# Performance work log

Measured on AMD Instinct MI355X. Metric: run time of the kernel, lower is better.

Reference implementation:

```python
import jax, jax.numpy as jnp
import numpy as np

B_SZ, SEQ, FEAT, STATE = 4, 4096, 1024, 64
HID = 4 * FEAT
EPS = 1e-5
LOG_DT_MIN, LOG_DT_MAX = float(np.log(0.001)), float(np.log(0.1))


def _s5_params(key, feat, state):
    ks = jax.random.split(key, 6)
    n = jnp.arange(state, dtype=jnp.float32)
    return {
        'log_A_real': jnp.log(n + 0.5),          # HiPPO-diag: A_real = -(n+0.5)
        'A_imag': jnp.pi * n,                     # HiPPO-diag: A_imag = pi*n
        'B_re': jax.random.normal(ks[0], (state, feat)) / np.sqrt(state),
        'B_im': jax.random.normal(ks[1], (state, feat)) / np.sqrt(state),
        'C_re': jax.random.normal(ks[2], (feat, state)) / np.sqrt(feat),
        'C_im': jax.random.normal(ks[3], (feat, state)) / np.sqrt(feat),
        'D': jax.random.normal(ks[4], (feat,)),
        'log_dt': jax.random.uniform(ks[5], (state,), minval=LOG_DT_MIN, maxval=LOG_DT_MAX),
    }


def setup_inputs() -> dict:
    key = jax.random.key(0)
    k = jax.random.split(key, 10)
    pf = _s5_params(k[2], FEAT, STATE)
    pb = _s5_params(k[3], FEAT, STATE)
    inp = {
        'x': jax.random.normal(k[0], (B_SZ, SEQ, FEAT), jnp.float32),
        'cond': jax.random.normal(k[1], (B_SZ, FEAT), jnp.float32),
        'ada_W': jax.random.normal(k[4], (FEAT, 6 * FEAT)) * 0.02,
        'ada_b': jnp.zeros((6 * FEAT,), jnp.float32),
        'out_W': jax.random.normal(k[5], (2 * FEAT, FEAT)) / np.sqrt(2 * FEAT),
        'out_b': jnp.zeros((FEAT,), jnp.float32),
        'mlp_W1': jax.random.normal(k[6], (FEAT, HID)) / np.sqrt(FEAT),
        'mlp_b1': jnp.zeros((HID,), jnp.float32),
        'mlp_W2': jax.random.normal(k[7], (HID, FEAT)) / np.sqrt(HID),
        'mlp_b2': jnp.zeros((FEAT,), jnp.float32),
        'freqs_cis': jnp.zeros((SEQ, STATE), jnp.float32),  # accepted, unused (interface compat)
    }
    for name, p in (('fwd', pf), ('bwd', pb)):
        for kk, v in p.items():
            inp[f'{name}_{kk}'] = v
    return inp


def _layernorm(x):
    # LayerNorm with use_scale=False, use_bias=False
    mu = jnp.mean(x, axis=-1, keepdims=True)
    var = jnp.var(x, axis=-1, keepdims=True)
    return (x - mu) * jax.lax.rsqrt(var + EPS)


def _s5(u, log_A_real, A_imag, B_re, B_im, C_re, C_im, D, log_dt):
    # Diagonal S5: x_k = A_bar*x_{k-1} + B_bar*u_k ; y = Re(C x) + D u
    dt = jnp.exp(log_dt)                                   # [N]
    A_diag = -jnp.exp(log_A_real) + 1j * A_imag            # [N] complex
    A_bar = jnp.exp(A_diag * dt)                           # [N]
    B_bar = (A_bar[:, None] - 1.0) / (A_diag[:, None] + 1e-8) * (B_re + 1j * B_im)  # [N,F]
    u_f = u.astype(jnp.float32)
    Bu = jnp.einsum('bsf,nf->bsn', u_f, B_bar)             # [B,S,N] complex
    A_exp = jnp.broadcast_to(A_bar[None, None, :], Bu.shape)

    def comb(e1, e2):
        a1, b1 = e1
        a2, b2 = e2
        return (a1 * a2, a2 * b1 + b2)

    _, xs = jax.lax.associative_scan(comb, (A_exp, Bu), axis=1)  # [B,S,N]
    y = jnp.einsum('fn,bsn->bsf', C_re + 1j * C_im, xs).real
    return y + D * u_f


def _block(x, cond, ada_W, ada_b, pf, pb, out_W, out_b, mlp_W1, mlp_b1, mlp_W2, mlp_b2):
    # AdaLN modulation params (standard DiT ordering: shift/scale/gate for msa then mlp)
    ada = jax.nn.silu(cond) @ ada_W + ada_b                # [B,6F]
    sh1, sc1, g1, sh2, sc2, g2 = jnp.split(ada, 6, axis=-1)
    h = _layernorm(x) * (1.0 + sc1[:, None, :]) + sh1[:, None, :]
    # bidirectional S5
    y_f = _s5(h, *pf)
    y_b = jnp.flip(_s5(jnp.flip(h, 1), *pb), 1)
    y = jnp.concatenate([y_f, y_b], axis=-1) @ out_W + out_b
    x = x + g1[:, None, :] * y
    h2 = _layernorm(x) * (1.0 + sc2[:, None, :]) + sh2[:, None, :]
    h2 = jax.nn.gelu(h2 @ mlp_W1 + mlp_b1) @ mlp_W2 + mlp_b2
    return x + g2[:, None, :] * h2


def reference(x, cond, ada_W, ada_b,
              fwd_log_A_real, fwd_A_imag, fwd_B_re, fwd_B_im, fwd_C_re, fwd_C_im, fwd_D, fwd_log_dt,
              bwd_log_A_real, bwd_A_imag, bwd_B_re, bwd_B_im, bwd_C_re, bwd_C_im, bwd_D, bwd_log_dt,
              out_W, out_b, mlp_W1, mlp_b1, mlp_W2, mlp_b2, freqs_cis):
    pf = (fwd_log_A_real, fwd_A_imag, fwd_B_re, fwd_B_im, fwd_C_re, fwd_C_im, fwd_D, fwd_log_dt)
    pb = (bwd_log_A_real, bwd_A_imag, bwd_B_re, bwd_B_im, bwd_C_re, bwd_C_im, bwd_D, bwd_log_dt)
    return _block(x, cond, ada_W, ada_b, pf, pb, out_W, out_b, mlp_W1, mlp_b1, mlp_W2, mlp_b2)
```

## Files before the change

kernel.cpp:

```cpp
#include <hip/hip_runtime.h>
#include <cstddef>

#define NF    1024
#define NSEQ  4096
#define NB    4
#define NROWS (NB*NSEQ)
#define NADA  6144
#define NHID  4096
#define NST   64
#define NCH   128
#define LCH   64
#define NCHUNK (NSEQ/LCH)
#define LDA   1280

typedef __bf16 bf16x8 __attribute__((ext_vector_type(8)));
typedef float f32x4 __attribute__((ext_vector_type(4)));

__device__ __forceinline__ unsigned short f2bf(float x) {
  union { float f; unsigned int u; } v; v.f = x;
  unsigned int r = v.u + 0x7fffu + ((v.u >> 16) & 1u);
  return (unsigned short)(r >> 16);
}

__device__ __forceinline__ float gelu_fast(float x) {
  float u2 = 1.5957691216057308f*(x + 0.044715f*x*x*x);
  return x / (1.f + __expf(-u2));
}

template<int TM, int TN, int WM, int WN>
__device__ __forceinline__ void mfma_core(
    const unsigned short* __restrict__ A, int lda,
    const unsigned short* __restrict__ Bt, int ldb,
    int K, int row0, int col0, unsigned short* lds, f32x4* acc)
{
  constexpr int MI = TM/(16*WM), NJ = TN/(16*WN);
  const int tid  = threadIdx.x;
  const int wave = tid >> 6, lane = tid & 63;
  const int wm = wave % WM, wn = wave / WM;
  const int sr = lane >> 2;
  const int sc = (lane & 3) << 3;
  const int fr = lane & 15, fq = lane >> 4;
  unsigned short* sA = lds;
  unsigned short* sB = lds + TM*32;
  const unsigned short* a0 = A + (size_t)row0*lda;
  const unsigned short* b0 = Bt + (size_t)col0*ldb;
#pragma unroll 2
  for (int k0 = 0; k0 < K; k0 += 32) {
#pragma unroll
    for (int s = 0; s < TM/64; ++s) {
      int u = s*4 + wave;
      int r = u*16 + sr;
      __builtin_amdgcn_global_load_lds(
          (const __attribute__((address_space(1))) void*)(a0 + (size_t)r*lda + k0 + sc),
          (__attribute__((address_space(3))) void*)(sA + u*512), 16, 0, 0);
    }
#pragma unroll
    for (int s = 0; s < TN/64; ++s) {
      int u = s*4 + wave;
      int r = u*16 + sr;
      __builtin_amdgcn_global_load_lds(
          (const __attribute__((address_space(1))) void*)(b0 + (size_t)r*ldb + k0 + sc),
          (__attribute__((address_space(3))) void*)(sB + u*512), 16, 0, 0);
    }
    __syncthreads();
    bf16x8 af[MI], bv[NJ];
#pragma unroll
    for (int i = 0; i < MI; ++i)
      af[i] = *(const bf16x8*)(sA + (wm*(MI*16) + i*16 + fr)*32 + fq*8);
#pragma unroll
    for (int j = 0; j < NJ; ++j)
      bv[j] = *(const bf16x8*)(sB + (wn*(NJ*16) + j*16 + fr)*32 + fq*8);
#pragma unroll
    for (int i = 0; i < MI; ++i)
#pragma unroll
      for (int j = 0; j < NJ; ++j)
        acc[i*NJ+j] = __builtin_amdgcn_mfma_f32_16x16x32_bf16(af[i], bv[j], acc[i*NJ+j], 0, 0, 0);
    __syncthreads();
  }
}

#define ACC_INIT(N_) f32x4 acc[N_]; \
  _Pragma("unroll") for (int z_ = 0; z_ < N_; ++z_) acc[z_] = (f32x4){0.f,0.f,0.f,0.f};

#define EPI_LOOP(WM_, MI_, NJ_, body) \
  { const int lane = threadIdx.x & 63, wave = threadIdx.x >> 6; \
    const int wm = wave % WM_, wn = wave / WM_; \
    const int fr = lane & 15, fq = lane >> 4; \
    _Pragma("unroll") for (int i = 0; i < MI_; ++i) \
    _Pragma("unroll") for (int j = 0; j < NJ_; ++j) \
    _Pragma("unroll") for (int r = 0; r < 4; ++r) { \
      int row = row0 + wm*(MI_*16) + i*16 + fq*4 + r; \
      int col = col0 + wn*(NJ_*16) + j*16 + fr; \
      float aval = acc[i*NJ_+j][r]; \
      body; } }

__global__ __launch_bounds__(256, 4) void k_mm_bu(const unsigned short* __restrict__ A,
                                                  const unsigned short* __restrict__ Bt,
                                                  float* __restrict__ C) {
  __shared__ __align__(16) unsigned short lds[(64+128)*32];
  ACC_INIT(8)
  int row0 = blockIdx.x*64, col0 = blockIdx.y*128;
  mfma_core<64,128,1,4>(A, LDA, Bt, 1024, 1024, row0, col0, lds, acc);
  EPI_LOOP(1, 4, 2, C[(size_t)row*(2*NCH) + col] = aval; )
}

__global__ __launch_bounds__(256, 4) void k_mm_g(const unsigned short* __restrict__ A,
                                                 const unsigned short* __restrict__ Bt,
                                                 unsigned short* __restrict__ Bcat) {
  __shared__ __align__(16) unsigned short lds[(64+128)*32];
  ACC_INIT(8)
  int row0 = blockIdx.x*64, col0 = blockIdx.y*128;
  mfma_core<64,128,1,4>(A, 2048, Bt, 2048, 2048, row0, col0, lds, acc);
  EPI_LOOP(1, 4, 2, Bcat[(size_t)col*LDA + row] = f2bf(aval); )
}

__global__ __launch_bounds__(256, 4) void k_mm_proj(const unsigned short* __restrict__ A,
                                                    const unsigned short* __restrict__ Bt,
                                                    const float* __restrict__ x,
                                                    const float* __restrict__ ada,
                                                    const float* __restrict__ outb,
                                                    float* __restrict__ outp) {
  __shared__ __align__(16) unsigned short lds[2*128*32];
  ACC_INIT(16)
  int row0 = blockIdx.x*128, col0 = blockIdx.y*128;
  mfma_core<128,128,2,2>(A, LDA, Bt, LDA, LDA, row0, col0, lds, acc);
  EPI_LOOP(2, 4, 4,
    const float* g1 = ada + (size_t)(row >> 12)*NADA + 2*NF;
    outp[(size_t)row*NF + col] = x[(size_t)row*NF + col] + g1[col]*(aval + outb[col]); )
}

__global__ __launch_bounds__(256, 4) void k_mm_mlp1(const unsigned short* __restrict__ A,
                                                    const unsigned short* __restrict__ Bt,
                                                    const float* __restrict__ b1,
                                                    unsigned short* __restrict__ mid) {
  __shared__ __align__(16) unsigned short lds[2*128*32];
  ACC_INIT(16)
  int row0 = blockIdx.x*128, col0 = blockIdx.y*128;
  mfma_core<128,128,2,2>(A, LDA, Bt, 1024, 1024, row0, col0, lds, acc);
  EPI_LOOP(2, 4, 4, mid[(size_t)row*NHID + col] = f2bf(gelu_fast(aval + b1[col])); )
}

__global__ __launch_bounds__(256, 4) void k_mm_mlp2(const unsigned short* __restrict__ A,
                                                    const unsigned short* __restrict__ Bt,
                                                    const float* __restrict__ b2,
                                                    const float* __restrict__ ada,
                                                    float* __restrict__ outp, int row_off) {
  __shared__ __align__(16) unsigned short lds[2*128*32];
  ACC_INIT(16)
  int row0 = blockIdx.x*128, col0 = blockIdx.y*128;
  mfma_core<128,128,2,2>(A, NHID, Bt, NHID, NHID, row0, col0, lds, acc);
  EPI_LOOP(2, 4, 4,
    int rg = row_off + row;
    const float* g2 = ada + (size_t)(rg >> 12)*NADA + 5*NF;
    outp[(size_t)rg*NF + col] += g2[col]*(aval + b2[col]); )
}

__global__ __launch_bounds__(256) void k_ada1(const float* __restrict__ cond, const float* __restrict__ adaW,
                                              float* __restrict__ part) {
  int j = blockIdx.x*256 + threadIdx.x;
  int b = blockIdx.y, z = blockIdx.z;
  float acc = 0.f;
  const float* s = cond + b*NF;
  int k0 = z*128;
  for (int k = k0; k < k0+128; ++k) {
    float c = s[k];
    acc += (c / (1.f + __expf(-c))) * adaW[(size_t)k*NADA + j];
  }
  part[((size_t)(z*NB + b))*NADA + j] = acc;
}

__global__ __launch_bounds__(256) void k_ada2(const float* __restrict__ part, const float* __restrict__ adab,
                                              float* __restrict__ ada) {
  int j = blockIdx.x*256 + threadIdx.x;
  int b = blockIdx.y;
  float acc = adab[j];
#pragma unroll
  for (int z = 0; z < 8; ++z) acc += part[((size_t)(z*NB + b))*NADA + j];
  ada[(size_t)b*NADA + j] = acc;
}

__global__ __launch_bounds__(64) void k_param(
    const float* __restrict__ lAf, const float* __restrict__ Aif, const float* __restrict__ ldtf,
    const float* __restrict__ lAb, const float* __restrict__ Aib, const float* __restrict__ ldtb,
    float* __restrict__ Abar, float* __restrict__ coef, float* __restrict__ AbarL, float* __restrict__ Apow)
{
  int d = blockIdx.x, n = threadIdx.x;
  const float* lA  = d ? lAb  : lAf;
  const float* Ai  = d ? Aib  : Aif;
  const float* ldt = d ? ldtb : ldtf;
  float dt  = expf(ldt[n]);
  float Are = -expf(lA[n]);
  float Aim = Ai[n];
  float ar = Are*dt, ai = Aim*dt;
  float m = expf(ar);
  float Abr = m*cosf(ai), Abi = m*sinf(ai);
  int t = d*NST + n;
  Abar[2*t] = Abr; Abar[2*t+1] = Abi;
  float cr = Abr - 1.f, ci = Abi;
  float dr = Are + 1e-8f, di = Aim;
  float den = dr*dr + di*di;
  coef[2*t]   = (cr*dr + ci*di)/den;
  coef[2*t+1] = (ci*dr - cr*di)/den;
  for (int j = 0; j < LCH; ++j) {
    float p = (float)(j+1);
    float mp = expf(ar*p);
    Apow[(size_t)(t*LCH + j)*2 + 0] = mp*cosf(ai*p);
    Apow[(size_t)(t*LCH + j)*2 + 1] = mp*sinf(ai*p);
  }
  float mL = expf(ar*64.f);
  AbarL[2*t] = mL*cosf(ai*64.f); AbarL[2*t+1] = mL*sinf(ai*64.f);
}

__global__ __launch_bounds__(256) void k_bmat_t(
    const float* __restrict__ Brf, const float* __restrict__ Bif,
    const float* __restrict__ Brb, const float* __restrict__ Bib,
    const float* __restrict__ coef, unsigned short* __restrict__ Bmat_t)
{
  int id = blockIdx.x*256 + threadIdx.x;
  int f = id & (NF-1), c = id >> 10;
  int d = c >> 6, n = c & 63;
  const float* Br = d ? Brb : Brf;
  const float* Bi = d ? Bib : Bif;
  float br = Br[(size_t)n*NF + f], bi = Bi[(size_t)n*NF + f];
  float crr = coef[2*c], cii = coef[2*c+1];
  Bmat_t[(size_t)(2*c)*NF + f]   = f2bf(crr*br - cii*bi);
  Bmat_t[(size_t)(2*c+1)*NF + f] = f2bf(crr*bi + cii*br);
}

__global__ __launch_bounds__(256) void k_ccat(
    const float* __restrict__ Crf, const float* __restrict__ Cif,
    const float* __restrict__ Crb, const float* __restrict__ Cib,
    unsigned short* __restrict__ Ccat)
{
  int id = blockIdx.x*256 + threadIdx.x;
  int fp = id & 2047, r = id >> 11;
  int p = r & 1, c = r >> 1, d = c >> 6, n = c & 63;
  int fd = fp >> 10, f = fp & 1023;
  float v = 0.f;
  if (fd == d) {
    const float* Cr = d ? Crb : Crf;
    const float* Ci = d ? Cib : Cif;
    v = p ? -Ci[(size_t)f*NST + n] : Cr[(size_t)f*NST + n];
  }
  Ccat[id] = f2bf(v);
}

__global__ __launch_bounds__(256) void k_ln_mod_bf(const float* __restrict__ xin, const float* __restrict__ ada,
                                                   int sh_off, int sc_off, unsigned short* __restrict__ outp) {
  const int row = blockIdx.x;
  const int b = row >> 12;
  const int tid = threadIdx.x;
  float4 v = ((const float4*)(xin + (size_t)row*NF))[tid];
  float s1 = v.x+v.y+v.z+v.w;
  float s2 = v.x*v.x + v.y*v.y + v.z*v.z + v.w*v.w;
  for (int off = 32; off > 0; off >>= 1) { s1 += __shfl_down(s1, off); s2 += __shfl_down(s2, off); }
  __shared__ float r1[4], r2[4];
  if ((tid & 63) == 0) { r1[tid>>6] = s1; r2[tid>>6] = s2; }
  __syncthreads();
  float S1 = r1[0]+r1[1]+r1[2]+r1[3];
  float S2 = r2[0]+r2[1]+r2[2]+r2[3];
  float mean = S1 * (1.0f/NF);
  float var  = S2 * (1.0f/NF) - mean*mean;
  float inv  = rsqrtf(var + 1e-5f);
  const float* arow = ada + (size_t)b*NADA;
  int f = tid << 2;
  ushort4 r;
  r.x = f2bf((v.x - mean)*inv*(1.f + arow[sc_off + f+0]) + arow[sh_off + f+0]);
  r.y = f2bf((v.y - mean)*inv*(1.f + arow[sc_off + f+1]) + arow[sh_off + f+1]);
  r.z = f2bf((v.z - mean)*inv*(1.f + arow[sc_off + f+2]) + arow[sh_off + f+2]);
  r.w = f2bf((v.w - mean)*inv*(1.f + arow[sc_off + f+3]) + arow[sh_off + f+3]);
  *(ushort4*)(outp + (size_t)row*LDA + f) = r;
}

__global__ __launch_bounds__(128) void k_scanA(float* __restrict__ Bu, const float* __restrict__ Abar,
                                               float* __restrict__ P) {
  int t = threadIdx.x;
  int bc = blockIdx.x;
  int b = bc >> 6, c = bc & 63;
  int d = t >> 6;
  float2 A = ((const float2*)Abar)[t];
  float sr = 0.f, si = 0.f;
  size_t base = ((size_t)b*NSEQ)*(2*NCH);
  for (int j = 0; j < LCH; ++j) {
    int s = d ? (c*LCH + (LCH-1) - j) : (c*LCH + j);
    float2* p = (float2*)(Bu + base + (size_t)s*(2*NCH)) + t;
    float2 u = *p;
    float nr = A.x*sr - A.y*si + u.x;
    float ni = A.x*si + A.y*sr + u.y;
    sr = nr; si = ni;
    *p = make_float2(sr, si);
  }
  ((float2*)P)[(size_t)bc*NCH + t] = make_float2(sr, si);
}

__global__ __launch_bounds__(512) void k_scanB(const float* __restrict__ P, const float* __restrict__ AbarL,
                                               float* __restrict__ carry) {
  int t = threadIdx.x & (NCH-1);
  int b = threadIdx.x >> 7;
  int d = t >> 6;
  float2 AL = ((const float2*)AbarL)[t];
  float sr = 0.f, si = 0.f;
  if (d == 0) {
    for (int c = 0; c < NCHUNK; ++c) {
      ((float2*)carry)[((size_t)b*NCHUNK + c)*NCH + t] = make_float2(sr, si);
      float2 p = ((const float2*)P)[((size_t)b*NCHUNK + c)*NCH + t];
      float nr = AL.x*sr - AL.y*si + p.x;
      float ni = AL.x*si + AL.y*sr + p.y;
      sr = nr; si = ni;
    }
  } else {
    for (int c = NCHUNK-1; c >= 0; --c) {
      ((float2*)carry)[((size_t)b*NCHUNK + c)*NCH + t] = make_float2(sr, si);
      float2 p = ((const float2*)P)[((size_t)b*NCHUNK + c)*NCH + t];
      float nr = AL.x*sr - AL.y*si + p.x;
      float ni = AL.x*si + AL.y*sr + p.y;
      sr = nr; si = ni;
    }
  }
}

__global__ __launch_bounds__(128) void k_scanC(const float* __restrict__ Bu, const float* __restrict__ Apow,
                                               const float* __restrict__ carry,
                                               unsigned short* __restrict__ Acat) {
  int t = threadIdx.x;
  int bc = blockIdx.x;
  int b = bc >> 6, c = bc & 63;
  int d = t >> 6;
  float2 E = ((const float2*)carry)[(size_t)bc*NCH + t];
  const float2* Ap = ((const float2*)Apow) + (size_t)t*LCH;
  size_t base = ((size_t)b*NSEQ)*(2*NCH);
  for (int j = 0; j < LCH; ++j) {
    int s = c*LCH + j;
    int tau = d ? (LCH-1 - j) : j;
    float2 ap = Ap[tau];
    float2 v = *((const float2*)(Bu + base + (size_t)s*(2*NCH)) + t);
    v.x += ap.x*E.x - ap.y*E.y;
    v.y += ap.x*E.y + ap.y*E.x;
    ushort2 o; o.x = f2bf(v.x); o.y = f2bf(v.y);
    *(ushort2*)(Acat + (size_t)(b*NSEQ + s)*LDA + 2*t) = o;
  }
}

__global__ void k_tcvt(const float* __restrict__ src, int R, int C,
                       unsigned short* __restrict__ dst, int ldd) {
  __shared__ float t[32][33];
  int c0 = blockIdx.x*32, r0 = blockIdx.y*32;
  for (int rr = threadIdx.y; rr < 32; rr += 8)
    t[rr][threadIdx.x] = src[(size_t)(r0+rr)*C + c0 + threadIdx.x];
  __syncthreads();
  for (int rr = threadIdx.y; rr < 32; rr += 8)
    dst[(size_t)(c0+rr)*ldd + r0 + threadIdx.x] = f2bf(t[threadIdx.x][rr]);
}

__global__ void k_wd_t(const float* __restrict__ Df, const float* __restrict__ Db,
                       const float* __restrict__ W, unsigned short* __restrict__ dst) {
  __shared__ float t1[32][33], t2[32][33];
  __shared__ float df[32], db[32];
  int fo0 = blockIdx.x*32, f0 = blockIdx.y*32;
  for (int rr = threadIdx.y; rr < 32; rr += 8) {
    t1[rr][threadIdx.x] = W[(size_t)(f0+rr)*NF + fo0 + threadIdx.x];
    t2[rr][threadIdx.x] = W[(size_t)(NF+f0+rr)*NF + fo0 + threadIdx.x];
  }
  if (threadIdx.y == 0) { df[threadIdx.x] = Df[f0+threadIdx.x]; db[threadIdx.x] = Db[f0+threadIdx.x]; }
  __syncthreads();
  for (int rr = threadIdx.y; rr < 32; rr += 8)
    dst[(size_t)(fo0+rr)*LDA + f0 + threadIdx.x] =
        f2bf(df[threadIdx.x]*t1[threadIdx.x][rr] + db[threadIdx.x]*t2[threadIdx.x][rr]);
}

extern "C" void kernel_launch(void* const* d_in, const int* in_sizes, int n_in,
                              void* d_out, int out_size, void* d_ws, size_t ws_size,
                              hipStream_t stream) {
  const bool sig = (in_sizes[4] == 64);
  const float* x    = (const float*)d_in[0];
  const float* cond = (const float*)d_in[1];
  const float* adaW = (const float*)d_in[2];
  const float* adab = (const float*)d_in[3];
  const int fwd0 = sig ? 4 : 11;
  const int bwd0 = sig ? 12 : 19;
  const float* outW = (const float*)d_in[sig ? 20 : 4];
  const float* outb = (const float*)d_in[sig ? 21 : 5];
  const float* W1   = (const float*)d_in[sig ? 22 : 6];
  const float* b1   = (const float*)d_in[sig ? 23 : 7];
  const float* W2   = (const float*)d_in[sig ? 24 : 8];
  const float* b2   = (const float*)d_in[sig ? 25 : 9];
  const float* lAf  = (const float*)d_in[fwd0+0];
  const float* Aif  = (const float*)d_in[fwd0+1];
  const float* Brf  = (const float*)d_in[fwd0+2];
  const float* Bif  = (const float*)d_in[fwd0+3];
  const float* Crf  = (const float*)d_in[fwd0+4];
  const float* Cif  = (const float*)d_in[fwd0+5];
  const float* Df   = (const float*)d_in[fwd0+6];
  const float* ldtf = (const float*)d_in[fwd0+7];
  const float* lAb  = (const float*)d_in[bwd0+0];
  const float* Aib  = (const float*)d_in[bwd0+1];
  const float* Brb  = (const float*)d_in[bwd0+2];
  const float* Bib  = (const float*)d_in[bwd0+3];
  const float* Crb  = (const float*)d_in[bwd0+4];
  const float* Cib  = (const float*)d_in[bwd0+5];
  const float* Db   = (const float*)d_in[bwd0+6];
  const float* ldtb = (const float*)d_in[bwd0+7];
  float* out = (float*)d_out;
  (void)n_in; (void)out_size;

  char* w = (char*)d_ws;
  auto alloc = [&](size_t bytes) { char* p = w; w += (bytes + 255) & ~(size_t)255; return p; };
  unsigned short* Acat   = (unsigned short*)alloc((size_t)NROWS*LDA*2);
  unsigned short* W1t    = (unsigned short*)alloc((size_t)NHID*NF*2);
  unsigned short* W2t    = (unsigned short*)alloc((size_t)NF*NHID*2);
  unsigned short* Wot    = (unsigned short*)alloc((size_t)NF*2048*2);
  unsigned short* Ccat   = (unsigned short*)alloc((size_t)256*2048*2);
  unsigned short* Bmat_t = (unsigned short*)alloc((size_t)2*NCH*NF*2);
  unsigned short* Bcat   = (unsigned short*)alloc((size_t)NF*LDA*2);
  float* bu    = (float*)alloc((size_t)NROWS*2*NCH*4);
  float* ada   = (float*)alloc((size_t)NB*NADA*4);
  float* part  = (float*)alloc((size_t)8*NB*NADA*4);
  float* Abar  = (float*)alloc(2*NCH*4);
  float* AbarL = (float*)alloc(2*NCH*4);
  float* coef  = (float*)alloc(2*NCH*4);
  float* Apow  = (float*)alloc((size_t)NCH*LCH*2*4);
  float* P     = (float*)alloc((size_t)NB*NCHUNK*NCH*2*4);
  float* carry = (float*)alloc((size_t)NB*NCHUNK*NCH*2*4);
  size_t used = (size_t)(w - (char*)d_ws);
  int mrows = NROWS;
  while (mrows > 4096 && used + (size_t)mrows*NHID*2 > ws_size) mrows >>= 1;
  unsigned short* mid = (unsigned short*)alloc((size_t)mrows*NHID*2);

  k_ada1<<<dim3(NADA/256, NB, 8), 256, 0, stream>>>(cond, adaW, part);
  k_ada2<<<dim3(NADA/256, NB), 256, 0, stream>>>(part, adab, ada);
  k_param<<<2, 64, 0, stream>>>(lAf, Aif, ldtf, lAb, Aib, ldtb, Abar, coef, AbarL, Apow);
  k_bmat_t<<<(2*NCH*NF)/(2*256), 256, 0, stream>>>(Brf, Bif, Brb, Bib, coef, Bmat_t);
  k_ccat<<<(256*2048)/256, 256, 0, stream>>>(Crf, Cif, Crb, Cib, Ccat);

  k_tcvt<<<dim3(NHID/32, NF/32), dim3(32,8), 0, stream>>>(W1, NF, NHID, W1t, NF);
  k_tcvt<<<dim3(NF/32, NHID/32), dim3(32,8), 0, stream>>>(W2, NHID, NF, W2t, NHID);
  k_tcvt<<<dim3(NF/32, 2048/32), dim3(32,8), 0, stream>>>(outW, 2048, NF, Wot, 2048);

  k_mm_g<<<dim3(4, NF/128), 256, 0, stream>>>(Ccat, Wot, Bcat);
  k_wd_t<<<dim3(NF/32, NF/32), dim3(32,8), 0, stream>>>(Df, Db, outW, Bcat + 256);

  k_ln_mod_bf<<<NROWS, 256, 0, stream>>>(x, ada, 0, NF, Acat + 256);

  k_mm_bu<<<dim3(NROWS/64, (2*NCH)/128), 256, 0, stream>>>(Acat + 256, Bmat_t, bu);

  k_scanA<<<NB*NCHUNK, NCH, 0, stream>>>(bu, Abar, P);
  k_scanB<<<1, 512, 0, stream>>>(P, AbarL, carry);
  k_scanC<<<NB*NCHUNK, NCH, 0, stream>>>(bu, Apow, carry, Acat);

  k_mm_proj<<<dim3(NROWS/128, NF/128), 256, 0, stream>>>(Acat, Bcat, x, ada, outb, out);

  k_ln_mod_bf<<<NROWS, 256, 0, stream>>>(out, ada, 3*NF, 4*NF, Acat + 256);

  for (int r0 = 0; r0 < NROWS; r0 += mrows) {
    k_mm_mlp1<<<dim3(mrows/128, NHID/128), 256, 0, stream>>>(Acat + 256 + (size_t)r0*LDA, W1t, b1, mid);
    k_mm_mlp2<<<dim3(mrows/128, NF/128), 256, 0, stream>>>(mid, W2t, b2, ada, out, r0);
  }
}
```

Baseline: 785.9 us.

## Fuse chunk scan into Bu GEMM, merge prep kernels, deepen GEMM K-step

The first phase of the chunked scan now runs inside the Bu GEMM epilogue. The block stages its 64x128 tile in shared memory, runs the intra-chunk recurrence there, and writes Bu and the chunk carries. This removes one global read-modify-write of Bu and a separate launch. The weight transpose/convert kernels and the B/C table kernels are each merged into a single launch. The shared MFMA core now loads two 32-wide K slices per barrier pair, halving synchronizations at the cost of doubled LDS per block, which may lower occupancy.

```diff
diff --git a/kernel.cpp b/kernel.cpp
--- a/kernel.cpp
+++ b/kernel.cpp
@@ -15,6 +15,9 @@
 
 typedef __bf16 bf16x8 __attribute__((ext_vector_type(8)));
 typedef float f32x4 __attribute__((ext_vector_type(4)));
+
+#define AS1 __attribute__((address_space(1)))
+#define AS3 __attribute__((address_space(3)))
 
 __device__ __forceinline__ unsigned short f2bf(float x) {
   union { float f; unsigned int u; } v; v.f = x;
@@ -41,40 +44,44 @@
   const int sc = (lane & 3) << 3;
   const int fr = lane & 15, fq = lane >> 4;
   unsigned short* sA = lds;
-  unsigned short* sB = lds + TM*32;
+  unsigned short* sB = lds + 2*TM*32;
   const unsigned short* a0 = A + (size_t)row0*lda;
   const unsigned short* b0 = Bt + (size_t)col0*ldb;
-#pragma unroll 2
-  for (int k0 = 0; k0 < K; k0 += 32) {
-#pragma unroll
-    for (int s = 0; s < TM/64; ++s) {
-      int u = s*4 + wave;
-      int r = u*16 + sr;
-      __builtin_amdgcn_global_load_lds(
-          (const __attribute__((address_space(1))) void*)(a0 + (size_t)r*lda + k0 + sc),
-          (__attribute__((address_space(3))) void*)(sA + u*512), 16, 0, 0);
-    }
-#pragma unroll
-    for (int s = 0; s < TN/64; ++s) {
-      int u = s*4 + wave;
-      int r = u*16 + sr;
-      __builtin_amdgcn_global_load_lds(
-          (const __attribute__((address_space(1))) void*)(b0 + (size_t)r*ldb + k0 + sc),
-          (__attribute__((address_space(3))) void*)(sB + u*512), 16, 0, 0);
+  for (int k0 = 0; k0 < K; k0 += 64) {
+#pragma unroll
+    for (int p = 0; p < 2; ++p) {
+      int kk = k0 + p*32;
+#pragma unroll
+      for (int s = 0; s < TM/64; ++s) {
+        int u = s*4 + wave;
+        __builtin_amdgcn_global_load_lds(
+            (const AS1 void*)(a0 + (size_t)(u*16 + sr)*lda + kk + sc),
+            (AS3 void*)(sA + p*TM*32 + u*512), 16, 0, 0);
+      }
+#pragma unroll
+      for (int s = 0; s < TN/64; ++s) {
+        int u = s*4 + wave;
+        __builtin_amdgcn_global_load_lds(
+            (const AS1 void*)(b0 + (size_t)(u*16 + sr)*ldb + kk + sc),
+            (AS3 void*)(sB + p*TN*32 + u*512), 16, 0, 0);
+      }
     }
     __syncthreads();
-    bf16x8 af[MI], bv[NJ];
-#pragma unroll
-    for (int i = 0; i < MI; ++i)
-      af[i] = *(const bf16x8*)(sA + (wm*(MI*16) + i*16 + fr)*32 + fq*8);
-#pragma unroll
-    for (int j = 0; j < NJ; ++j)
-      bv[j] = *(const bf16x8*)(sB + (wn*(NJ*16) + j*16 + fr)*32 + fq*8);
-#pragma unroll
-    for (int i = 0; i < MI; ++i)
+#pragma unroll
+    for (int p = 0; p < 2; ++p) {
+      bf16x8 af[MI], bv[NJ];
+#pragma unroll
+      for (int i = 0; i < MI; ++i)
+        af[i] = *(const bf16x8*)(sA + p*TM*32 + (wm*(MI*16) + i*16 + fr)*32 + fq*8);
 #pragma unroll
       for (int j = 0; j < NJ; ++j)
-        acc[i*NJ+j] = __builtin_amdgcn_mfma_f32_16x16x32_bf16(af[i], bv[j], acc[i*NJ+j], 0, 0, 0);
+        bv[j] = *(const bf16x8*)(sB + p*TN*32 + (wn*(NJ*16) + j*16 + fr)*32 + fq*8);
+#pragma unroll
+      for (int i = 0; i < MI; ++i)
+#pragma unroll
+        for (int j = 0; j < NJ; ++j)
+          acc[i*NJ+j] = __builtin_amdgcn_mfma_f32_16x16x32_bf16(af[i], bv[j], acc[i*NJ+j], 0, 0, 0);
+    }
     __syncthreads();
   }
 }
@@ -94,20 +101,60 @@
       float aval = acc[i*NJ_+j][r]; \
       body; } }
 
-__global__ __launch_bounds__(256, 4) void k_mm_bu(const unsigned short* __restrict__ A,
-                                                  const unsigned short* __restrict__ Bt,
-                                                  float* __restrict__ C) {
-  __shared__ __align__(16) unsigned short lds[(64+128)*32];
+__global__ __launch_bounds__(256, 4) void k_mm_bu_scan(
+    const unsigned short* __restrict__ A, const unsigned short* __restrict__ Bt,
+    const float* __restrict__ Abar, float* __restrict__ Bu, float* __restrict__ P)
+{
+  __shared__ __align__(16) char smem[64*128*4];
+  unsigned short* lds = (unsigned short*)smem;
+  float* sbuf = (float*)smem;
   ACC_INIT(8)
   int row0 = blockIdx.x*64, col0 = blockIdx.y*128;
   mfma_core<64,128,1,4>(A, LDA, Bt, 1024, 1024, row0, col0, lds, acc);
-  EPI_LOOP(1, 4, 2, C[(size_t)row*(2*NCH) + col] = aval; )
+  { const int lane = threadIdx.x & 63, wave = threadIdx.x >> 6;
+    const int fr = lane & 15, fq = lane >> 4;
+#pragma unroll
+    for (int i = 0; i < 4; ++i)
+#pragma unroll
+      for (int j = 0; j < 2; ++j)
+#pragma unroll
+        for (int r = 0; r < 4; ++r) {
+          int rl = i*16 + fq*4 + r;
+          int cl = wave*32 + j*16 + fr;
+          sbuf[rl*128 + cl] = acc[i*2+j][r];
+        }
+  }
+  __syncthreads();
+  int tid = threadIdx.x;
+  if (tid < 64) {
+    int ch = (col0 >> 1) + tid;
+    int d = ch >> 6;
+    float2 Ae = ((const float2*)Abar)[ch];
+    float sr_ = 0.f, si_ = 0.f;
+    for (int jj = 0; jj < LCH; ++jj) {
+      int rl = d ? (LCH-1 - jj) : jj;
+      float re = sbuf[rl*128 + 2*tid];
+      float im = sbuf[rl*128 + 2*tid + 1];
+      float nr = Ae.x*sr_ - Ae.y*si_ + re;
+      float ni = Ae.x*si_ + Ae.y*sr_ + im;
+      sr_ = nr; si_ = ni;
+      sbuf[rl*128 + 2*tid]     = sr_;
+      sbuf[rl*128 + 2*tid + 1] = si_;
+    }
+    int bc = row0 >> 6;
+    ((float2*)P)[(size_t)bc*NCH + ch] = make_float2(sr_, si_);
+  }
+  __syncthreads();
+  for (int e = tid; e < 64*32; e += 256) {
+    int r = e >> 5, q = (e & 31) << 2;
+    *(float4*)(Bu + (size_t)(row0 + r)*(2*NCH) + col0 + q) = *(float4*)(sbuf + r*128 + q);
+  }
 }
 
 __global__ __launch_bounds__(256, 4) void k_mm_g(const unsigned short* __restrict__ A,
                                                  const unsigned short* __restrict__ Bt,
                                                  unsigned short* __restrict__ Bcat) {
-  __shared__ __align__(16) unsigned short lds[(64+128)*32];
+  __shared__ __align__(16) unsigned short lds[2*(64+128)*32];
   ACC_INIT(8)
   int row0 = blockIdx.x*64, col0 = blockIdx.y*128;
   mfma_core<64,128,1,4>(A, 2048, Bt, 2048, 2048, row0, col0, lds, acc);
@@ -120,7 +167,7 @@
                                                     const float* __restrict__ ada,
                                                     const float* __restrict__ outb,
                                                     float* __restrict__ outp) {
-  __shared__ __align__(16) unsigned short lds[2*128*32];
+  __shared__ __align__(16) unsigned short lds[2*2*128*32];
   ACC_INIT(16)
   int row0 = blockIdx.x*128, col0 = blockIdx.y*128;
   mfma_core<128,128,2,2>(A, LDA, Bt, LDA, LDA, row0, col0, lds, acc);
@@ -133,7 +180,7 @@
                                                     const unsigned short* __restrict__ Bt,
                                                     const float* __restrict__ b1,
                                                     unsigned short* __restrict__ mid) {
-  __shared__ __align__(16) unsigned short lds[2*128*32];
+  __shared__ __align__(16) unsigned short lds[2*2*128*32];
   ACC_INIT(16)
   int row0 = blockIdx.x*128, col0 = blockIdx.y*128;
   mfma_core<128,128,2,2>(A, LDA, Bt, 1024, 1024, row0, col0, lds, acc);
@@ -145,7 +192,7 @@
                                                     const float* __restrict__ b2,
                                                     const float* __restrict__ ada,
                                                     float* __restrict__ outp, int row_off) {
-  __shared__ __align__(16) unsigned short lds[2*128*32];
+  __shared__ __align__(16) unsigned short lds[2*2*128*32];
   ACC_INIT(16)
   int row0 = blockIdx.x*128, col0 = blockIdx.y*128;
   mfma_core<128,128,2,2>(A, NHID, Bt, NHID, NHID, row0, col0, lds, acc);
@@ -211,38 +258,81 @@
   AbarL[2*t] = mL*cosf(ai*64.f); AbarL[2*t+1] = mL*sinf(ai*64.f);
 }
 
-__global__ __launch_bounds__(256) void k_bmat_t(
+__global__ __launch_bounds__(256) void k_tabs(
     const float* __restrict__ Brf, const float* __restrict__ Bif,
     const float* __restrict__ Brb, const float* __restrict__ Bib,
-    const float* __restrict__ coef, unsigned short* __restrict__ Bmat_t)
-{
-  int id = blockIdx.x*256 + threadIdx.x;
-  int f = id & (NF-1), c = id >> 10;
-  int d = c >> 6, n = c & 63;
-  const float* Br = d ? Brb : Brf;
-  const float* Bi = d ? Bib : Bif;
-  float br = Br[(size_t)n*NF + f], bi = Bi[(size_t)n*NF + f];
-  float crr = coef[2*c], cii = coef[2*c+1];
-  Bmat_t[(size_t)(2*c)*NF + f]   = f2bf(crr*br - cii*bi);
-  Bmat_t[(size_t)(2*c+1)*NF + f] = f2bf(crr*bi + cii*br);
-}
-
-__global__ __launch_bounds__(256) void k_ccat(
+    const float* __restrict__ coef, unsigned short* __restrict__ Bmat_t,
     const float* __restrict__ Crf, const float* __restrict__ Cif,
     const float* __restrict__ Crb, const float* __restrict__ Cib,
     unsigned short* __restrict__ Ccat)
 {
-  int id = blockIdx.x*256 + threadIdx.x;
-  int fp = id & 2047, r = id >> 11;
-  int p = r & 1, c = r >> 1, d = c >> 6, n = c & 63;
-  int fd = fp >> 10, f = fp & 1023;
-  float v = 0.f;
-  if (fd == d) {
-    const float* Cr = d ? Crb : Crf;
-    const float* Ci = d ? Cib : Cif;
-    v = p ? -Ci[(size_t)f*NST + n] : Cr[(size_t)f*NST + n];
-  }
-  Ccat[id] = f2bf(v);
+  if (blockIdx.x < 512) {
+    int id = blockIdx.x*256 + threadIdx.x;
+    int f = id & (NF-1), c = id >> 10;
+    int d = c >> 6, n = c & 63;
+    const float* Br = d ? Brb : Brf;
+    const float* Bi = d ? Bib : Bif;
+    float br = Br[(size_t)n*NF + f], bi = Bi[(size_t)n*NF + f];
+    float crr = coef[2*c], cii = coef[2*c+1];
+    Bmat_t[(size_t)(2*c)*NF + f]   = f2bf(crr*br - cii*bi);
+    Bmat_t[(size_t)(2*c+1)*NF + f] = f2bf(crr*bi + cii*br);
+  } else {
+    int id = (blockIdx.x - 512)*256 + threadIdx.x;
+    int fp = id & 2047, r = id >> 11;
+    int p = r & 1, c = r >> 1, d = c >> 6, n = c & 63;
+    int fd = fp >> 10, f = fp & 1023;
+    float v = 0.f;
+    if (fd == d) {
+      const float* Cr = d ? Crb : Crf;
+      const float* Ci = d ? Cib : Cif;
+      v = p ? -Ci[(size_t)f*NST + n] : Cr[(size_t)f*NST + n];
+    }
+    Ccat[id] = f2bf(v);
+  }
+}
+
+__device__ __forceinline__ void tcvt_tile(const float* __restrict__ src, int C,
+                                          unsigned short* __restrict__ dst, int ldd,
+                                          int r0, int c0, float* t) {
+  for (int rr = threadIdx.y; rr < 32; rr += 8)
+    t[rr*33 + threadIdx.x] = src[(size_t)(r0+rr)*C + c0 + threadIdx.x];
+  __syncthreads();
+  for (int rr = threadIdx.y; rr < 32; rr += 8)
+    dst[(size_t)(c0+rr)*ldd + r0 + threadIdx.x] = f2bf(t[threadIdx.x*33 + rr]);
+}
+
+__global__ void k_wprep(const float* __restrict__ W1, const float* __restrict__ W2,
+                        const float* __restrict__ outW,
+                        const float* __restrict__ Df, const float* __restrict__ Db,
+                        unsigned short* __restrict__ W1t, unsigned short* __restrict__ W2t,
+                        unsigned short* __restrict__ Wot, unsigned short* __restrict__ BcatWD) {
+  __shared__ float t1[32*33], t2[32*33];
+  __shared__ float df[32], db[32];
+  int g = blockIdx.x;
+  if (g < 4096) {
+    int c0 = (g & 127)*32, r0 = (g >> 7)*32;
+    tcvt_tile(W1, NHID, W1t, NF, r0, c0, t1);
+  } else if (g < 8192) {
+    int g2 = g - 4096;
+    int c0 = (g2 & 31)*32, r0 = (g2 >> 5)*32;
+    tcvt_tile(W2, NF, W2t, NHID, r0, c0, t1);
+  } else if (g < 10240) {
+    int g3 = g - 8192;
+    int c0 = (g3 & 31)*32, r0 = (g3 >> 5)*32;
+    tcvt_tile(outW, NF, Wot, 2048, r0, c0, t1);
+  } else {
+    int g4 = g - 10240;
+    int fo0 = (g4 & 31)*32, f0 = (g4 >> 5)*32;
+    for (int rr = threadIdx.y; rr < 32; rr += 8) {
+      t1[rr*33 + threadIdx.x] = outW[(size_t)(f0+rr)*NF + fo0 + threadIdx.x];
+      t2[rr*33 + threadIdx.x] = outW[(size_t)(NF+f0+rr)*NF + fo0 + threadIdx.x];
+    }
+    if (threadIdx.y == 0) { df[threadIdx.x] = Df[f0+threadIdx.x]; db[threadIdx.x] = Db[f0+threadIdx.x]; }
+    __syncthreads();
+    for (int rr = threadIdx.y; rr < 32; rr += 8)
+      BcatWD[(size_t)(fo0+rr)*LDA + f0 + threadIdx.x] =
+          f2bf(df[threadIdx.x]*t1[threadIdx.x*33 + rr] + db[threadIdx.x]*t2[threadIdx.x*33 + rr]);
+  }
 }
 
 __global__ __launch_bounds__(256) void k_ln_mod_bf(const float* __restrict__ xin, const float* __restrict__ ada,
@@ -272,27 +362,6 @@
   *(ushort4*)(outp + (size_t)row*LDA + f) = r;
 }
 
-__global__ __launch_bounds__(128) void k_scanA(float* __restrict__ Bu, const float* __restrict__ Abar,
-                                               float* __restrict__ P) {
-  int t = threadIdx.x;
-  int bc = blockIdx.x;
-  int b = bc >> 6, c = bc & 63;
-  int d = t >> 6;
-  float2 A = ((const float2*)Abar)[t];
-  float sr = 0.f, si = 0.f;
-  size_t base = ((size_t)b*NSEQ)*(2*NCH);
-  for (int j = 0; j < LCH; ++j) {
-    int s = d ? (c*LCH + (LCH-1) - j) : (c*LCH + j);
-    float2* p = (float2*)(Bu + base + (size_t)s*(2*NCH)) + t;
-    float2 u = *p;
-    float nr = A.x*sr - A.y*si + u.x;
-    float ni = A.x*si + A.y*sr + u.y;
-    sr = nr; si = ni;
-    *p = make_float2(sr, si);
-  }
-  ((float2*)P)[(size_t)bc*NCH + t] = make_float2(sr, si);
-}
-
 __global__ __launch_bounds__(512) void k_scanB(const float* __restrict__ P, const float* __restrict__ AbarL,
                                                float* __restrict__ carry) {
   int t = threadIdx.x & (NCH-1);
@@ -339,33 +408,6 @@
     ushort2 o; o.x = f2bf(v.x); o.y = f2bf(v.y);
     *(ushort2*)(Acat + (size_t)(b*NSEQ + s)*LDA + 2*t) = o;
   }
-}
-
-__global__ void k_tcvt(const float* __restrict__ src, int R, int C,
-                       unsigned short* __restrict__ dst, int ldd) {
-  __shared__ float t[32][33];
-  int c0 = blockIdx.x*32, r0 = blockIdx.y*32;
-  for (int rr = threadIdx.y; rr < 32; rr += 8)
-    t[rr][threadIdx.x] = src[(size_t)(r0+rr)*C + c0 + threadIdx.x];
-  __syncthreads();
-  for (int rr = threadIdx.y; rr < 32; rr += 8)
-    dst[(size_t)(c0+rr)*ldd + r0 + threadIdx.x] = f2bf(t[threadIdx.x][rr]);
-}
-
-__global__ void k_wd_t(const float* __restrict__ Df, const float* __restrict__ Db,
-                       const float* __restrict__ W, unsigned short* __restrict__ dst) {
-  __shared__ float t1[32][33], t2[32][33];
-  __shared__ float df[32], db[32];
-  int fo0 = blockIdx.x*32, f0 = blockIdx.y*32;
-  for (int rr = threadIdx.y; rr < 32; rr += 8) {
-    t1[rr][threadIdx.x] = W[(size_t)(f0+rr)*NF + fo0 + threadIdx.x];
-    t2[rr][threadIdx.x] = W[(size_t)(NF+f0+rr)*NF + fo0 + threadIdx.x];
-  }
-  if (threadIdx.y == 0) { df[threadIdx.x] = Df[f0+threadIdx.x]; db[threadIdx.x] = Db[f0+threadIdx.x]; }
-  __syncthreads();
-  for (int rr = threadIdx.y; rr < 32; rr += 8)
-    dst[(size_t)(fo0+rr)*LDA + f0 + threadIdx.x] =
-        f2bf(df[threadIdx.x]*t1[threadIdx.x][rr] + db[threadIdx.x]*t2[threadIdx.x][rr]);
 }
 
 extern "C" void kernel_launch(void* const* d_in, const int* in_sizes, int n_in,
@@ -429,21 +471,15 @@
   k_ada1<<<dim3(NADA/256, NB, 8), 256, 0, stream>>>(cond, adaW, part);
   k_ada2<<<dim3(NADA/256, NB), 256, 0, stream>>>(part, adab, ada);
   k_param<<<2, 64, 0, stream>>>(lAf, Aif, ldtf, lAb, Aib, ldtb, Abar, coef, AbarL, Apow);
-  k_bmat_t<<<(2*NCH*NF)/(2*256), 256, 0, stream>>>(Brf, Bif, Brb, Bib, coef, Bmat_t);
-  k_ccat<<<(256*2048)/256, 256, 0, stream>>>(Crf, Cif, Crb, Cib, Ccat);
-
-  k_tcvt<<<dim3(NHID/32, NF/32), dim3(32,8), 0, stream>>>(W1, NF, NHID, W1t, NF);
-  k_tcvt<<<dim3(NF/32, NHID/32), dim3(32,8), 0, stream>>>(W2, NHID, NF, W2t, NHID);
-  k_tcvt<<<dim3(NF/32, 2048/32), dim3(32,8), 0, stream>>>(outW, 2048, NF, Wot, 2048);
+  k_tabs<<<2560, 256, 0, stream>>>(Brf, Bif, Brb, Bib, coef, Bmat_t, Crf, Cif, Crb, Cib, Ccat);
+  k_wprep<<<11264, dim3(32,8), 0, stream>>>(W1, W2, outW, Df, Db, W1t, W2t, Wot, Bcat + 256);
 
   k_mm_g<<<dim3(4, NF/128), 256, 0, stream>>>(Ccat, Wot, Bcat);
-  k_wd_t<<<dim3(NF/32, NF/32), dim3(32,8), 0, stream>>>(Df, Db, outW, Bcat + 256);
 
   k_ln_mod_bf<<<NROWS, 256, 0, stream>>>(x, ada, 0, NF, Acat + 256);
 
-  k_mm_bu<<<dim3(NROWS/64, (2*NCH)/128), 256, 0, stream>>>(Acat + 256, Bmat_t, bu);
-
-  k_scanA<<<NB*NCHUNK, NCH, 0, stream>>>(bu, Abar, P);
+  k_mm_bu_scan<<<dim3(NROWS/64, (2*NCH)/128), 256, 0, stream>>>(Acat + 256, Bmat_t, Abar, bu, P);
+
   k_scanB<<<1, 512, 0, stream>>>(P, AbarL, carry);
   k_scanC<<<NB*NCHUNK, NCH, 0, stream>>>(bu, Apow, carry, Acat);
 
```

After: 765.9 us. 1.03x faster.
